# Kernel optimization log

Measured on AMD Instinct MI355X. Metric: run time of the kernel, lower is better.

Reference implementation:

```python
import jax, jax.numpy as jnp
import numpy as np

D, DFFN, H, P, L = 256, 1024, 8, 4, 4
B, LQ = 32, 300
LENS = [2048, 1024, 512, 256]
STARTS = [0, 2048, 3072, 3584]
S = sum(LENS)


def setup_inputs() -> dict:
    key = jax.random.key(0)
    ks = iter(jax.random.split(key, 64))
    def W(shape, s=0.02):
        return jax.random.normal(next(ks), shape, jnp.float32) * s
    inp = {}
    inp['tgt'] = W((B, LQ, D), 1.0)
    inp['query_pos'] = W((B, LQ, D), 1.0)
    centers = jax.random.uniform(next(ks), (B, LQ, L))
    widths = 0.05 + 0.2 * jax.random.uniform(next(ks), (B, LQ, L))
    inp['reference_points'] = jnp.stack([centers, widths], -1)  # (B,Lq,L,2) = (center,width)
    inp['src'] = W((B, S, D), 1.0)
    inp['temporal_lengths'] = np.array(LENS, np.int64)
    inp['level_start_index'] = np.array(STARTS, np.int64)
    for n, shape in [('sa_qw', (D, D)), ('sa_kw', (D, D)), ('sa_vw', (D, D)), ('sa_ow', (D, D)), ('ff1_w', (D, DFFN)), ('ff2_w', (DFFN, D))]:
        inp[n] = W(shape)
    for n, sz in [('sa_qb', D), ('sa_kb', D), ('sa_vb', D), ('sa_ob', D), ('ff1_b', DFFN), ('ff2_b', D)]:
        inp[n] = jnp.zeros((sz,), jnp.float32)
    for pre in ['ca', 'se']:
        inp[pre + '_off_w'] = W((D, H * L * P))
        inp[pre + '_off_b'] = jnp.zeros((H * L * P,), jnp.float32)
        inp[pre + '_attn_w'] = W((D, H * L * P))
        inp[pre + '_attn_b'] = jnp.zeros((H * L * P,), jnp.float32)
        inp[pre + '_val_w'] = W((D, D))
        inp[pre + '_val_b'] = jnp.zeros((D,), jnp.float32)
        inp[pre + '_out_w'] = W((D, D))
        inp[pre + '_out_b'] = jnp.zeros((D,), jnp.float32)
    for n in ['ln1', 'lnse', 'ln2', 'ln3']:
        inp[n + '_g'] = jnp.ones((D,), jnp.float32)
        inp[n + '_b'] = jnp.zeros((D,), jnp.float32)
    return inp


def _ln(x, g, b, eps=1e-5):
    m = jnp.mean(x, -1, keepdims=True)
    v = jnp.mean((x - m) ** 2, -1, keepdims=True)
    return (x - m) * jax.lax.rsqrt(v + eps) * g + b


def _mha(q, k, v, qw, qb, kw, kb, vw, vb, ow, ob):
    b, lq, d = q.shape
    dh = d // H
    qh = (q @ qw + qb).reshape(b, lq, H, dh).transpose(0, 2, 1, 3)
    kh = (k @ kw + kb).reshape(b, -1, H, dh).transpose(0, 2, 1, 3)
    vh = (v @ vw + vb).reshape(b, -1, H, dh).transpose(0, 2, 1, 3)
    scores = jnp.einsum('bhqd,bhkd->bhqk', qh, kh) * (dh ** -0.5)
    attn = jax.nn.softmax(scores, -1)
    out = jnp.einsum('bhqk,bhkd->bhqd', attn, vh).transpose(0, 2, 1, 3).reshape(b, lq, d)
    return out @ ow + ob


def _deform(q, ref, src, lens, starts, vw, vb, offw, offb, aw, ab, ow, ob, boundary):
    b, lq, d = q.shape
    dh = d // H
    value = (src @ vw + vb).reshape(b, -1, H, dh)  # (B,S,H,Dh)
    off = (q @ offw + offb).reshape(b, lq, H, L, P)
    attn = jax.nn.softmax((q @ aw + ab).reshape(b, lq, H, L * P), -1).reshape(b, lq, H, L, P)
    center = ref[..., 0][:, :, None, :, None]  # (B,Lq,1,L,1)
    width = ref[..., 1][:, :, None, :, None]
    if boundary:
        # half the points anchored at segment start, half at segment end
        sign = jnp.where(jnp.arange(P) < P // 2, -0.5, 0.5)
        anchor = center + sign * width
    else:
        anchor = center
    loc = anchor + off / P * width * 0.5  # normalized sampling locations (B,Lq,H,L,P)
    out = jnp.zeros((b, lq, H, dh), value.dtype)
    for l in range(L):
        T = int(lens[l]); s0 = int(starts[l])
        v = value[:, s0:s0 + T].transpose(0, 2, 1, 3)  # (B,H,T,Dh)
        x = loc[:, :, :, l, :] * T - 0.5  # align_corners=False grid
        x0 = jnp.floor(x)
        w = x - x0
        i0 = x0.astype(jnp.int32)
        i1 = i0 + 1
        m0 = ((i0 >= 0) & (i0 < T)).astype(v.dtype)
        m1 = ((i1 >= 0) & (i1 < T)).astype(v.dtype)
        i0c = jnp.clip(i0, 0, T - 1)
        i1c = jnp.clip(i1, 0, T - 1)
        def gather(idx):
            idxh = idx.transpose(0, 2, 1, 3).reshape(b, H, lq * P, 1)
            g = jnp.take_along_axis(v, jnp.broadcast_to(idxh, (b, H, lq * P, dh)), axis=2)
            return g.reshape(b, H, lq, P, dh).transpose(0, 2, 1, 3, 4)  # (B,Lq,H,P,Dh)
        samp = gather(i0c) * ((1 - w) * m0)[..., None] + gather(i1c) * (w * m1)[..., None]
        out = out + jnp.einsum('bqhp,bqhpd->bqhd', attn[:, :, :, l, :], samp)
    return out.reshape(b, lq, d) @ ow + ob


def reference(tgt, query_pos, reference_points, src, temporal_lengths, level_start_index,
              sa_qw, sa_qb, sa_kw, sa_kb, sa_vw, sa_vb, sa_ow, sa_ob,
              ca_off_w, ca_off_b, ca_attn_w, ca_attn_b, ca_val_w, ca_val_b, ca_out_w, ca_out_b,
              se_off_w, se_off_b, se_attn_w, se_attn_b, se_val_w, se_val_b, se_out_w, se_out_b,
              ff1_w, ff1_b, ff2_w, ff2_b,
              ln1_g, ln1_b, lnse_g, lnse_b, ln2_g, ln2_b, ln3_g, ln3_b):
    lens = np.asarray(temporal_lengths)
    starts = np.asarray(level_start_index)
    q = tgt + query_pos
    t2 = _mha(q, q, tgt, sa_qw, sa_qb, sa_kw, sa_kb, sa_vw, sa_vb, sa_ow, sa_ob)
    tgt = _ln(tgt + t2, ln2_g, ln2_b)
    t2 = _deform(tgt + query_pos, reference_points, src, lens, starts,
                 ca_val_w, ca_val_b, ca_off_w, ca_off_b, ca_attn_w, ca_attn_b, ca_out_w, ca_out_b, False)
    tgt = _ln(tgt + t2, ln1_g, ln1_b)
    t2 = _deform(tgt + query_pos, reference_points, src, lens, starts,
                 se_val_w, se_val_b, se_off_w, se_off_b, se_attn_w, se_attn_b, se_out_w, se_out_b, True)
    tgt = _ln(tgt + t2, lnse_g, lnse_b)
    t2 = jax.nn.relu(tgt @ ff1_w + ff1_b) @ ff2_w + ff2_b
    tgt = _ln(tgt + t2, ln3_g, ln3_b)
    return tgt
```

## Files before the change

### kernel.cpp

```cpp
#include <hip/hip_runtime.h>
#include <hip/hip_bf16.h>

namespace {

typedef unsigned short u16;
typedef unsigned int u32;

constexpr int D    = 256;
constexpr int H    = 8;
constexpr int DH   = 32;
constexpr int B    = 32;
constexpr int LQ   = 300;
constexpr int NQ   = B * LQ;
constexpr int S    = 3840;
constexpr int MS   = B * S;
constexpr int DFFN = 1024;

typedef __attribute__((ext_vector_type(8))) short bf16x8;
typedef __attribute__((ext_vector_type(4))) float f32x4;

__device__ inline u16 f2b(float x) {
  u32 u = __builtin_bit_cast(u32, x);
  u32 r = (u + 0x7FFFu + ((u >> 16) & 1u)) >> 16;
  return (u16)r;
}
__device__ inline u32 pk2(float a, float b) {
  return (u32)f2b(a) | ((u32)f2b(b) << 16);
}
__device__ inline void unpack2(u32 w, float& a, float& b) {
  a = __builtin_bit_cast(float, w << 16);
  b = __builtin_bit_cast(float, w & 0xffff0000u);
}

template<bool BOUNDARY>
__device__ inline void deform_phase(
    int tid, int m0,
    const float* __restrict__ oa, const float* __restrict__ ref,
    const u16* __restrict__ value, uint4* owt , char* Ast)
{
#pragma unroll
  for (int qq = 0; qq < 8; ++qq) {
    const int ql = (tid >> 7) + 4 * qq;
    const int bq = m0 + ql;
    const int t  = tid & 127;
    const int h = t >> 4;
    const int l = (t >> 2) & 3;
    const int p = t & 3;

    const float off    = oa[(size_t)bq * 256 + t];
    const float logit  = oa[(size_t)bq * 256 + 128 + t];
    const float center = ref[(size_t)bq * 8 + l * 2 + 0];
    const float width  = ref[(size_t)bq * 8 + l * 2 + 1];

    const float e = __expf(logit);
    float ssum = e;
    ssum += __shfl_xor(ssum, 1, 64);
    ssum += __shfl_xor(ssum, 2, 64);
    ssum += __shfl_xor(ssum, 4, 64);
    ssum += __shfl_xor(ssum, 8, 64);
    const float wa = e / ssum;

    const int T  = 2048 >> l;
    const int s0 = 4096 - (4096 >> l);
    float anchor = center;
    if (BOUNDARY) anchor += (p < 2 ? -0.5f : 0.5f) * width;
    const float loc = anchor + off * width * 0.125f;
    const float x = loc * (float)T - 0.5f;
    const float x0 = floorf(x);
    const float w = x - x0;
    const int i0 = (int)x0;
    const int i1 = i0 + 1;
    const float w0 = (i0 >= 0 && i0 < T) ? wa * (1.f - w) : 0.f;
    const float w1 = (i1 >= 0 && i1 < T) ? wa * w : 0.f;
    const int i0c = min(max(i0, 0), T - 1);
    const int i1c = min(max(i1, 0), T - 1);
    uint4 pack;
    pack.x = (u32)((h * S + s0 + i0c) * (DH * 2));
    pack.y = __builtin_bit_cast(u32, w0);
    pack.z = (u32)((h * S + s0 + i1c) * (DH * 2));
    pack.w = __builtin_bit_cast(u32, w1);
    owt[ql * 128 + t] = pack;
  }
  __syncthreads();

#pragma unroll
  for (int qq = 0; qq < 8; ++qq) {
    const int ql = (tid >> 7) + 4 * qq;
    const int bq = m0 + ql;
    const int b = bq / LQ;
    const int t = tid & 127;
    const int g  = t >> 4;
    const int ln = t & 15;
    const int qd = ln & 3;
    const int ts = ln >> 2;
    const char* vb = (const char*)(value + (size_t)b * H * S * DH) + qd * 16;
    float o[8] = {};
#pragma unroll
    for (int i = 0; i < 8; ++i) {
      const int rowidx = i * 4 + ts;
      const uint4 ow = owt[ql * 128 + g * 16 + (rowidx >> 1)];
      const u32 boff = (rowidx & 1) ? ow.z : ow.x;
      const float wt = __builtin_bit_cast(float, (rowidx & 1) ? ow.w : ow.y);
      const uint4 v = *(const uint4*)(vb + boff);
      float a0, a1;
      unpack2(v.x, a0, a1); o[0] += wt * a0; o[1] += wt * a1;
      unpack2(v.y, a0, a1); o[2] += wt * a0; o[3] += wt * a1;
      unpack2(v.z, a0, a1); o[4] += wt * a0; o[5] += wt * a1;
      unpack2(v.w, a0, a1); o[6] += wt * a0; o[7] += wt * a1;
    }
#pragma unroll
    for (int d = 0; d < 8; ++d) {
      o[d] += __shfl_xor(o[d], 4, 64);
      o[d] += __shfl_xor(o[d], 8, 64);
    }
    if (ts == 0) {
      const int col = g * DH + qd * 8;
      uint4 wv;
      wv.x = pk2(o[0], o[1]); wv.y = pk2(o[2], o[3]);
      wv.z = pk2(o[4], o[5]); wv.w = pk2(o[6], o[7]);
      *(uint4*)(Ast + ql * 512 + ((col * 2) ^ ((ql & 7) << 4))) = wv;
    }
  }
  __syncthreads();
}

__global__ __launch_bounds__(256) void gemm_qkv(
    const u16* __restrict__ qbuf, const u16* __restrict__ tgtb,
    const u16* __restrict__ saqk_t, const u16* __restrict__ sav_t,
    const float* __restrict__ qkb, const float* __restrict__ vbias,
    u16* __restrict__ qkbuf, u16* __restrict__ vh)
{
  constexpr int K = 256, BK = 64, LDK = 72;
  __shared__ __align__(16) u16 sh[128 * LDK];
  u16* As = sh;
  u16* Bs = sh + 64 * LDK;
  const bool isv = blockIdx.x >= 8;
  const u16* A  = isv ? tgtb : qbuf;
  const u16* Bt = isv ? sav_t : saqk_t;
  const float* bias = isv ? vbias : qkb;
  u16* C = isv ? vh : qkbuf;
  const int N = isv ? 256 : 512;
  const int n0 = (isv ? (int)blockIdx.x - 8 : (int)blockIdx.x) * 64;
  const int m0 = blockIdx.y * 64;

  const int tid  = threadIdx.x;
  const int lane = tid & 63;
  const int wid  = tid >> 6;
  const int wm = wid >> 1, wn = wid & 1;

  f32x4 acc[2][2] = {};
  uint4 ra[2], rb[2];
  const int srow = tid >> 3, sch = (tid & 7) * 8;

#pragma unroll
  for (int i = 0; i < 2; ++i) {
    const int row = srow + i * 32;
    ra[i] = *(const uint4*)(A  + (size_t)(m0 + row) * K + sch);
    rb[i] = *(const uint4*)(Bt + (size_t)(n0 + row) * K + sch);
  }
  for (int t = 0; t < 4; ++t) {
#pragma unroll
    for (int i = 0; i < 2; ++i) {
      const int row = srow + i * 32;
      *(uint4*)(&As[row * LDK + sch]) = ra[i];
      *(uint4*)(&Bs[row * LDK + sch]) = rb[i];
    }
    __syncthreads();
    if (t + 1 < 4) {
      const int k0 = (t + 1) * BK;
#pragma unroll
      for (int i = 0; i < 2; ++i) {
        const int row = srow + i * 32;
        ra[i] = *(const uint4*)(A  + (size_t)(m0 + row) * K + k0 + sch);
        rb[i] = *(const uint4*)(Bt + (size_t)(n0 + row) * K + k0 + sch);
      }
    }
#pragma unroll
    for (int kk = 0; kk < 2; ++kk) {
      const int krd = kk * 32 + (lane >> 4) * 8;
      bf16x8 af[2], bf[2];
#pragma unroll
      for (int m = 0; m < 2; ++m)
        af[m] = *(const bf16x8*)(&As[(wm * 32 + (lane & 15) + 16 * m) * LDK + krd]);
#pragma unroll
      for (int n = 0; n < 2; ++n)
        bf[n] = *(const bf16x8*)(&Bs[(wn * 32 + (lane & 15) + 16 * n) * LDK + krd]);
#pragma unroll
      for (int m = 0; m < 2; ++m)
#pragma unroll
        for (int n = 0; n < 2; ++n)
          acc[m][n] = __builtin_amdgcn_mfma_f32_16x16x32_bf16(af[m], bf[n], acc[m][n], 0, 0, 0);
    }
    __syncthreads();
  }

  const int cr = (lane >> 4) * 4;
  const int cc = lane & 15;
  u16* stg = sh;
#pragma unroll
  for (int n = 0; n < 2; ++n) {
    const int lc = wn * 32 + n * 16 + cc;
    const float bv = bias[n0 + lc];
#pragma unroll
    for (int m = 0; m < 2; ++m) {
      const int lr0 = wm * 32 + m * 16 + cr;
#pragma unroll
      for (int r = 0; r < 4; ++r)
        stg[(lr0 + r) * LDK + lc] = f2b(acc[m][n][r] + bv);
    }
  }
  __syncthreads();
#pragma unroll
  for (int i = 0; i < 2; ++i) {
    const int c = tid + 256 * i;
    const int row = c >> 3, ch = c & 7;
    *(uint4*)(C + (size_t)(m0 + row) * N + n0 + ch * 8) =
        *(const uint4*)(&stg[row * LDK + ch * 8]);
  }
}

__global__ __launch_bounds__(512) void gemm_val4(
    const float* __restrict__ A, const u16* __restrict__ Bt2,
    const float* __restrict__ bias2, u16* __restrict__ Vca, u16* __restrict__ Vse)
{
  __shared__ __align__(16) char shraw[33792];
  char* Asw = shraw;
  const int tid  = threadIdx.x;
  const int lane = tid & 63;
  const int w    = tid >> 6;
  const int bid  = blockIdx.x;
  const int nh   = (bid >> 3) & 1;
  const int m0   = ((bid >> 4) * 8 + (bid & 7)) * 64;
  u16* dst = nh ? Vse : Vca;
  const u16* Bt = Bt2 + nh * 256 * 256;
  const float* bias = bias2 + nh * 256;
  const int b  = m0 / S;
  const int s0 = m0 - b * S;

#pragma unroll
  for (int i = 0; i < 4; ++i) {
    const int idx = tid + 512 * i;
    const int row = idx >> 5, ch = idx & 31;
    const float* ap = A + (size_t)(m0 + row) * 256 + ch * 8;
    const float4 f0 = *(const float4*)(ap);
    const float4 f1 = *(const float4*)(ap + 4);
    uint4 pk;
    pk.x = pk2(f0.x, f0.y); pk.y = pk2(f0.z, f0.w);
    pk.z = pk2(f1.x, f1.y); pk.w = pk2(f1.z, f1.w);
    *(uint4*)(Asw + row * 512 + ((ch * 16) ^ ((row & 7) << 4))) = pk;
  }
  __syncthreads();

  f32x4 acc[4][2] = {};
  const u16* bb = Bt + (size_t)(w * 32 + (lane & 15)) * 256 + (lane >> 4) * 8;
  bf16x8 bcur[2], bnxt[2];
#pragma unroll
  for (int n = 0; n < 2; ++n) bcur[n] = *(const bf16x8*)(bb + n * 4096);

#pragma unroll
  for (int kk = 0; kk < 8; ++kk) {
    bf16x8 af[4];
    const int kb = kk * 64 + (lane >> 4) * 16;
#pragma unroll
    for (int m = 0; m < 4; ++m) {
      const int row = m * 16 + (lane & 15);
      af[m] = *(const bf16x8*)(Asw + row * 512 + (kb ^ ((row & 7) << 4)));
    }
    if (kk < 7) {
#pragma unroll
      for (int n = 0; n < 2; ++n)
        bnxt[n] = *(const bf16x8*)(bb + n * 4096 + (kk + 1) * 32);
    }
#pragma unroll
    for (int m = 0; m < 4; ++m)
#pragma unroll
      for (int n = 0; n < 2; ++n)
        acc[m][n] = __builtin_amdgcn_mfma_f32_16x16x32_bf16(af[m], bcur[n], acc[m][n], 0, 0, 0);
#pragma unroll
    for (int n = 0; n < 2; ++n) bcur[n] = bnxt[n];
  }
  __syncthreads();

  constexpr int STC = 264;
  u16* stg = (u16*)shraw;
  const int cr = (lane >> 4) * 4;
  const int cc = lane & 15;
#pragma unroll
  for (int n = 0; n < 2; ++n) {
    const int col = w * 32 + n * 16 + cc;
    const float bv = bias[col];
#pragma unroll
    for (int m = 0; m < 4; ++m) {
      const int r0 = m * 16 + cr;
#pragma unroll
      for (int r = 0; r < 4; ++r)
        stg[(r0 + r) * STC + col] = f2b(acc[m][n][r] + bv);
    }
  }
  __syncthreads();
  u16* vb = dst + (size_t)b * H * S * DH;
#pragma unroll
  for (int i = 0; i < 4; ++i) {
    const int c = tid + 512 * i;
    const int row = c >> 5, ch = c & 31;
    const int h = ch >> 2, dq = ch & 3;
    *(uint4*)(vb + ((size_t)h * S + (s0 + row)) * DH + dq * 8) =
        *(const uint4*)(&stg[row * STC + ch * 8]);
  }
}

__global__ __launch_bounds__(1024) void gemm_lnoff(
    const u16* __restrict__ A, const u16* __restrict__ Bt,
    const float* __restrict__ bias, const float* __restrict__ res,
    const float* __restrict__ g, const float* __restrict__ be,
    const float* __restrict__ qpos,
    const u16* __restrict__ offw, const float* __restrict__ offb,
    float* __restrict__ fout, float* __restrict__ oaout)
{
  constexpr int K = 256, LDK = 72;
  __shared__ __align__(16) float ftile[64 * 264];
  u16* As = (u16*)ftile;
  u16* Bs = As + 64 * LDK;
  u16* aq = (u16*)ftile;
  const int tid  = threadIdx.x;
  const int lane = tid & 63;
  const int wid  = tid >> 6;
  const int wm = wid >> 2, wn = wid & 3;
  const int m0 = blockIdx.x * 64;

  f32x4 acc[4] = {};
  const bool am = tid < 512;
  const int arow = tid >> 3, ach = (tid & 7) * 8;

  uint4 ra = {};
  uint4 rb[2];
  if (am) ra = *(const uint4*)(A + (size_t)(m0 + arow) * K + ach);
#pragma unroll
  for (int i = 0; i < 2; ++i) {
    const int idx = tid + 1024 * i;
    const int brow = idx >> 3, bch = (idx & 7) * 8;
    rb[i] = *(const uint4*)(Bt + (size_t)brow * K + bch);
  }

  for (int t = 0; t < 4; ++t) {
    if (am) *(uint4*)(&As[arow * LDK + ach]) = ra;
#pragma unroll
    for (int i = 0; i < 2; ++i) {
      const int idx = tid + 1024 * i;
      const int brow = idx >> 3, bch = (idx & 7) * 8;
      *(uint4*)(&Bs[brow * LDK + bch]) = rb[i];
    }
    __syncthreads();
    if (t + 1 < 4) {
      const int k0 = (t + 1) * 64;
      if (am) ra = *(const uint4*)(A + (size_t)(m0 + arow) * K + k0 + ach);
#pragma unroll
      for (int i = 0; i < 2; ++i) {
        const int idx = tid + 1024 * i;
        const int brow = idx >> 3, bch = (idx & 7) * 8;
        rb[i] = *(const uint4*)(Bt + (size_t)brow * K + k0 + bch);
      }
    }
#pragma unroll
    for (int kk = 0; kk < 2; ++kk) {
      const int krd = kk * 32 + (lane >> 4) * 8;
      bf16x8 af, bf[4];
      af = *(const bf16x8*)(&As[(wm * 16 + (lane & 15)) * LDK + krd]);
#pragma unroll
      for (int n = 0; n < 4; ++n)
        bf[n] = *(const bf16x8*)(&Bs[(wn * 64 + n * 16 + (lane & 15)) * LDK + krd]);
#pragma unroll
      for (int n = 0; n < 4; ++n)
        acc[n] = __builtin_amdgcn_mfma_f32_16x16x32_bf16(af, bf[n], acc[n], 0, 0, 0);
    }
    __syncthreads();
  }

  const int cr = (lane >> 4) * 4;
  const int cc = lane & 15;
#pragma unroll
  for (int n = 0; n < 4; ++n) {
    const int col = wn * 64 + n * 16 + cc;
    const float bv = bias[col];
#pragma unroll
    for (int r = 0; r < 4; ++r)
      ftile[(wm * 16 + cr + r) * 264 + col] = acc[n][r] + bv;
  }
  __syncthreads();

  const int row = tid >> 4, s16 = tid & 15;
  const size_t grow = (size_t)(m0 + row) * 256;
  float vv[16];
  float sum = 0.f;
#pragma unroll
  for (int j = 0; j < 4; ++j) {
    const int col = s16 * 4 + j * 64;
    const float4 fv = *(const float4*)(&ftile[row * 264 + col]);
    const float4 rv = *(const float4*)(res + grow + col);
    vv[j * 4 + 0] = fv.x + rv.x; vv[j * 4 + 1] = fv.y + rv.y;
    vv[j * 4 + 2] = fv.z + rv.z; vv[j * 4 + 3] = fv.w + rv.w;
    sum += vv[j * 4 + 0] + vv[j * 4 + 1] + vv[j * 4 + 2] + vv[j * 4 + 3];
  }
  sum += __shfl_xor(sum, 1, 64);
  sum += __shfl_xor(sum, 2, 64);
  sum += __shfl_xor(sum, 4, 64);
  sum += __shfl_xor(sum, 8, 64);
  const float mean = sum * (1.f / 256.f);
  float sq = 0.f;
#pragma unroll
  for (int k = 0; k < 16; ++k) { const float d = vv[k] - mean; sq += d * d; }
  sq += __shfl_xor(sq, 1, 64);
  sq += __shfl_xor(sq, 2, 64);
  sq += __shfl_xor(sq, 4, 64);
  sq += __shfl_xor(sq, 8, 64);
  const float rstd = rsqrtf(sq * (1.f / 256.f) + 1e-5f);

  float yq[16];
#pragma unroll
  for (int j = 0; j < 4; ++j) {
    const int col = s16 * 4 + j * 64;
    const float4 gv = *(const float4*)(g + col);
    const float4 bv = *(const float4*)(be + col);
    const float4 qv = *(const float4*)(qpos + grow + col);
    float4 y;
    y.x = (vv[j * 4 + 0] - mean) * rstd * gv.x + bv.x;
    y.y = (vv[j * 4 + 1] - mean) * rstd * gv.y + bv.y;
    y.z = (vv[j * 4 + 2] - mean) * rstd * gv.z + bv.z;
    y.w = (vv[j * 4 + 3] - mean) * rstd * gv.w + bv.w;
    *(float4*)(fout + grow + col) = y;
    yq[j * 4 + 0] = y.x + qv.x; yq[j * 4 + 1] = y.y + qv.y;
    yq[j * 4 + 2] = y.z + qv.z; yq[j * 4 + 3] = y.w + qv.w;
  }
  __syncthreads();

#pragma unroll
  for (int j = 0; j < 4; ++j) {
    const int col = s16 * 4 + j * 64;
    uint2 pk;
    pk.x = pk2(yq[j * 4 + 0], yq[j * 4 + 1]);
    pk.y = pk2(yq[j * 4 + 2], yq[j * 4 + 3]);
    *(uint2*)(&aq[row * 264 + col]) = pk;
  }
  __syncthreads();

  f32x4 acc2[4] = {};
  const u16* bb = offw + (size_t)(wn * 64 + (lane & 15)) * 256 + (lane >> 4) * 8;
#pragma unroll
  for (int kk = 0; kk < 8; ++kk) {
    const bf16x8 af = *(const bf16x8*)(&aq[(wm * 16 + (lane & 15)) * 264 + kk * 32 + (lane >> 4) * 8]);
#pragma unroll
    for (int n = 0; n < 4; ++n) {
      const bf16x8 bf = *(const bf16x8*)(bb + (size_t)n * 16 * 256 + kk * 32);
      acc2[n] = __builtin_amdgcn_mfma_f32_16x16x32_bf16(af, bf, acc2[n], 0, 0, 0);
    }
  }
  __syncthreads();

#pragma unroll
  for (int n = 0; n < 4; ++n) {
    const int col = wn * 64 + n * 16 + cc;
    const float bv = offb[col];
#pragma unroll
    for (int r = 0; r < 4; ++r)
      ftile[(wm * 16 + cr + r) * 264 + col] = acc2[n][r] + bv;
  }
  __syncthreads();
#pragma unroll
  for (int i = 0; i < 4; ++i) {
    const int c = tid + 1024 * i;
    const int rw = c >> 6, ch = c & 63;
    *(float4*)(oaout + (size_t)(m0 + rw) * 256 + ch * 4) =
        *(const float4*)(&ftile[rw * 264 + ch * 4]);
  }
}

__global__ __launch_bounds__(512) void deform_lnoff(
    const float* __restrict__ oa, const float* __restrict__ ref,
    const u16* __restrict__ value,
    const u16* __restrict__ Wout, const float* __restrict__ bout,
    const float* __restrict__ res, const float* __restrict__ g,
    const float* __restrict__ be, const float* __restrict__ qpos,
    const u16* __restrict__ offw, const float* __restrict__ offb,
    float* __restrict__ fout, float* __restrict__ oaout)
{
  __shared__ __align__(16) char sh[81920];
  char* Ast = sh;
  uint4* owt = (uint4*)(sh + 16384);
  float* ftile = (float*)sh;
  u16* aq = (u16*)sh;
  const int tid  = threadIdx.x;
  const int lane = tid & 63;
  const int w    = tid >> 6;
  const int m0   = blockIdx.x * 32;
  const int cr = (lane >> 4) * 4;
  const int cc = lane & 15;

  deform_phase<false>(tid, m0, oa, ref, value, owt, Ast);

  f32x4 accB[2][2] = {};
  {
    const u16* bb = Wout + (size_t)(w * 32 + (lane & 15)) * 256 + (lane >> 4) * 8;
#pragma unroll
    for (int kk = 0; kk < 8; ++kk) {
      bf16x8 af[2];
      const int kb = kk * 64 + (lane >> 4) * 16;
#pragma unroll
      for (int m = 0; m < 2; ++m) {
        const int row = m * 16 + (lane & 15);
        af[m] = *(const bf16x8*)(Ast + row * 512 + (kb ^ ((row & 7) << 4)));
      }
#pragma unroll
      for (int n = 0; n < 2; ++n) {
        const bf16x8 bf = *(const bf16x8*)(bb + (size_t)n * 16 * 256 + kk * 32);
#pragma unroll
        for (int m = 0; m < 2; ++m)
          accB[m][n] = __builtin_amdgcn_mfma_f32_16x16x32_bf16(af[m], bf, accB[m][n], 0, 0, 0);
      }
    }
  }
  __syncthreads();

#pragma unroll
  for (int n = 0; n < 2; ++n) {
    const int col = w * 32 + n * 16 + cc;
    const float bv = bout[col];
#pragma unroll
    for (int m = 0; m < 2; ++m)
#pragma unroll
      for (int r = 0; r < 4; ++r)
        ftile[(m * 16 + cr + r) * 264 + col] = accB[m][n][r] + bv;
  }
  __syncthreads();

  const int row = tid >> 4, s16 = tid & 15;
  const size_t grow = (size_t)(m0 + row) * 256;
  float yq[16];
  {
    float vv[16];
    float sum = 0.f;
#pragma unroll
    for (int j = 0; j < 4; ++j) {
      const int col = s16 * 4 + j * 64;
      const float4 fv = *(const float4*)(&ftile[row * 264 + col]);
      const float4 rv = *(const float4*)(res + grow + col);
      vv[j * 4 + 0] = fv.x + rv.x; vv[j * 4 + 1] = fv.y + rv.y;
      vv[j * 4 + 2] = fv.z + rv.z; vv[j * 4 + 3] = fv.w + rv.w;
      sum += vv[j * 4 + 0] + vv[j * 4 + 1] + vv[j * 4 + 2] + vv[j * 4 + 3];
    }
    sum += __shfl_xor(sum, 1, 64);
    sum += __shfl_xor(sum, 2, 64);
    sum += __shfl_xor(sum, 4, 64);
    sum += __shfl_xor(sum, 8, 64);
    const float mean = sum * (1.f / 256.f);
    float sq = 0.f;
#pragma unroll
    for (int k = 0; k < 16; ++k) { const float d = vv[k] - mean; sq += d * d; }
    sq += __shfl_xor(sq, 1, 64);
    sq += __shfl_xor(sq, 2, 64);
    sq += __shfl_xor(sq, 4, 64);
    sq += __shfl_xor(sq, 8, 64);
    const float rstd = rsqrtf(sq * (1.f / 256.f) + 1e-5f);
#pragma unroll
    for (int j = 0; j < 4; ++j) {
      const int col = s16 * 4 + j * 64;
      const float4 gv = *(const float4*)(g + col);
      const float4 bv = *(const float4*)(be + col);
      const float4 qv = *(const float4*)(qpos + grow + col);
      float4 y;
      y.x = (vv[j * 4 + 0] - mean) * rstd * gv.x + bv.x;
      y.y = (vv[j * 4 + 1] - mean) * rstd * gv.y + bv.y;
      y.z = (vv[j * 4 + 2] - mean) * rstd * gv.z + bv.z;
      y.w = (vv[j * 4 + 3] - mean) * rstd * gv.w + bv.w;
      *(float4*)(fout + grow + col) = y;
      yq[j * 4 + 0] = y.x + qv.x; yq[j * 4 + 1] = y.y + qv.y;
      yq[j * 4 + 2] = y.z + qv.z; yq[j * 4 + 3] = y.w + qv.w;
    }
  }
  __syncthreads();

#pragma unroll
  for (int j = 0; j < 4; ++j) {
    const int col = s16 * 4 + j * 64;
    uint2 pk;
    pk.x = pk2(yq[j * 4 + 0], yq[j * 4 + 1]);
    pk.y = pk2(yq[j * 4 + 2], yq[j * 4 + 3]);
    *(uint2*)(&aq[row * 264 + col]) = pk;
  }
  __syncthreads();

  f32x4 acc2[2][2] = {};
  {
    const u16* bb = offw + (size_t)(w * 32 + (lane & 15)) * 256 + (lane >> 4) * 8;
#pragma unroll
    for (int kk = 0; kk < 8; ++kk) {
      bf16x8 af[2];
#pragma unroll
      for (int m = 0; m < 2; ++m)
        af[m] = *(const bf16x8*)(&aq[(m * 16 + (lane & 15)) * 264 + kk * 32 + (lane >> 4) * 8]);
#pragma unroll
      for (int n = 0; n < 2; ++n) {
        const bf16x8 bf = *(const bf16x8*)(bb + (size_t)n * 16 * 256 + kk * 32);
#pragma unroll
        for (int m = 0; m < 2; ++m)
          acc2[m][n] = __builtin_amdgcn_mfma_f32_16x16x32_bf16(af[m], bf, acc2[m][n], 0, 0, 0);
      }
    }
  }
  __syncthreads();

#pragma unroll
  for (int n = 0; n < 2; ++n) {
    const int col = w * 32 + n * 16 + cc;
    const float bv = offb[col];
#pragma unroll
    for (int m = 0; m < 2; ++m)
#pragma unroll
      for (int r = 0; r < 4; ++r)
        ftile[(m * 16 + cr + r) * 264 + col] = acc2[m][n][r] + bv;
  }
  __syncthreads();
#pragma unroll
  for (int i = 0; i < 4; ++i) {
    const int c = tid + 512 * i;
    const int rw = c >> 6, ch = c & 63;
    *(float4*)(oaout + (size_t)(m0 + rw) * 256 + ch * 4) =
        *(const float4*)(&ftile[rw * 264 + ch * 4]);
  }
}

__global__ __launch_bounds__(512) void gemm_tail2(
    const float* __restrict__ oa, const float* __restrict__ ref,
    const u16* __restrict__ value,
    const u16* __restrict__ Wout, const float* __restrict__ bout,
    const float* __restrict__ res,
    const float* __restrict__ g1, const float* __restrict__ be1,
    const u16* __restrict__ B1t, const u16* __restrict__ B2t,
    const float* __restrict__ b1, const float* __restrict__ b2,
    const float* __restrict__ g2, const float* __restrict__ be2,
    float* __restrict__ fout)
{
  __shared__ __align__(16) char sh[81920];
  char* Ast = sh;
  uint4* owt = (uint4*)(sh + 16384);
  char* ffh = sh + 16384;
  float* ftile = (float*)sh;
  const int tid  = threadIdx.x;
  const int lane = tid & 63;
  const int w    = tid >> 6;
  const int m0   = blockIdx.x * 32;
  const int cr = (lane >> 4) * 4;
  const int cc = lane & 15;

  deform_phase<true>(tid, m0, oa, ref, value, owt, Ast);

  f32x4 accB[2][2] = {};
  {
    const u16* bb = Wout + (size_t)(w * 32 + (lane & 15)) * 256 + (lane >> 4) * 8;
#pragma unroll
    for (int kk = 0; kk < 8; ++kk) {
      bf16x8 af[2];
      const int kb = kk * 64 + (lane >> 4) * 16;
#pragma unroll
      for (int m = 0; m < 2; ++m) {
        const int row = m * 16 + (lane & 15);
        af[m] = *(const bf16x8*)(Ast + row * 512 + (kb ^ ((row & 7) << 4)));
      }
#pragma unroll
      for (int n = 0; n < 2; ++n) {
        const bf16x8 bf = *(const bf16x8*)(bb + (size_t)n * 16 * 256 + kk * 32);
#pragma unroll
        for (int m = 0; m < 2; ++m)
          accB[m][n] = __builtin_amdgcn_mfma_f32_16x16x32_bf16(af[m], bf, accB[m][n], 0, 0, 0);
      }
    }
  }
  __syncthreads();

#pragma unroll
  for (int n = 0; n < 2; ++n) {
    const int col = w * 32 + n * 16 + cc;
    const float bv = bout[col];
#pragma unroll
    for (int m = 0; m < 2; ++m)
#pragma unroll
      for (int r = 0; r < 4; ++r)
        ftile[(m * 16 + cr + r) * 264 + col] = accB[m][n][r] + bv;
  }
  __syncthreads();

  const int row = tid >> 4, s16 = tid & 15;
  const size_t grow = (size_t)(m0 + row) * 256;
  float yv[16];
  {
    float vv[16];
    float sum = 0.f;
#pragma unroll
    for (int j = 0; j < 4; ++j) {
      const int col = s16 * 4 + j * 64;
      const float4 fv = *(const float4*)(&ftile[row * 264 + col]);
      const float4 rv = *(const float4*)(res + grow + col);
      vv[j * 4 + 0] = fv.x + rv.x; vv[j * 4 + 1] = fv.y + rv.y;
      vv[j * 4 + 2] = fv.z + rv.z; vv[j * 4 + 3] = fv.w + rv.w;
      sum += vv[j * 4 + 0] + vv[j * 4 + 1] + vv[j * 4 + 2] + vv[j * 4 + 3];
    }
    sum += __shfl_xor(sum, 1, 64);
    sum += __shfl_xor(sum, 2, 64);
    sum += __shfl_xor(sum, 4, 64);
    sum += __shfl_xor(sum, 8, 64);
    const float mean = sum * (1.f / 256.f);
    float sq = 0.f;
#pragma unroll
    for (int k = 0; k < 16; ++k) { const float d = vv[k] - mean; sq += d * d; }
    sq += __shfl_xor(sq, 1, 64);
    sq += __shfl_xor(sq, 2, 64);
    sq += __shfl_xor(sq, 4, 64);
    sq += __shfl_xor(sq, 8, 64);
    const float rstd = rsqrtf(sq * (1.f / 256.f) + 1e-5f);
#pragma unroll
    for (int j = 0; j < 4; ++j) {
      const int col = s16 * 4 + j * 64;
      const float4 gv = *(const float4*)(g1 + col);
      const float4 bv = *(const float4*)(be1 + col);
      yv[j * 4 + 0] = (vv[j * 4 + 0] - mean) * rstd * gv.x + bv.x;
      yv[j * 4 + 1] = (vv[j * 4 + 1] - mean) * rstd * gv.y + bv.y;
      yv[j * 4 + 2] = (vv[j * 4 + 2] - mean) * rstd * gv.z + bv.z;
      yv[j * 4 + 3] = (vv[j * 4 + 3] - mean) * rstd * gv.w + bv.w;
    }
  }
  __syncthreads();

#pragma unroll
  for (int j = 0; j < 4; ++j) {
    const int col = s16 * 4 + j * 64;
    uint2 pk;
    pk.x = pk2(yv[j * 4 + 0], yv[j * 4 + 1]);
    pk.y = pk2(yv[j * 4 + 2], yv[j * 4 + 3]);
    *(uint2*)(Ast + row * 512 + ((col * 2) ^ ((row & 7) << 4))) = pk;
  }
  __syncthreads();

  {
    f32x4 acc[2][8] = {};
    const u16* bb = B1t + (size_t)(w * 128 + (lane & 15)) * 256 + (lane >> 4) * 8;
#pragma unroll
    for (int kk = 0; kk < 8; ++kk) {
      bf16x8 af[2];
      const int kb = kk * 64 + (lane >> 4) * 16;
#pragma unroll
      for (int m = 0; m < 2; ++m) {
        const int rw = m * 16 + (lane & 15);
        af[m] = *(const bf16x8*)(Ast + rw * 512 + (kb ^ ((rw & 7) << 4)));
      }
#pragma unroll
      for (int n = 0; n < 8; ++n) {
        const bf16x8 bf = *(const bf16x8*)(bb + (size_t)n * 16 * 256 + kk * 32);
#pragma unroll
        for (int m = 0; m < 2; ++m)
          acc[m][n] = __builtin_amdgcn_mfma_f32_16x16x32_bf16(af[m], bf, acc[m][n], 0, 0, 0);
      }
    }
#pragma unroll
    for (int n = 0; n < 8; ++n) {
      const int col = w * 128 + n * 16 + cc;
      const float bv = b1[col];
#pragma unroll
      for (int m = 0; m < 2; ++m) {
#pragma unroll
        for (int r = 0; r < 4; ++r) {
          const int rw = m * 16 + cr + r;
          const float x = fmaxf(acc[m][n][r] + bv, 0.f);
          *(u16*)(ffh + rw * 2048 + ((col * 2) ^ ((rw & 7) << 4))) = f2b(x);
        }
      }
    }
  }
  __syncthreads();

  f32x4 acc2[2][2] = {};
  {
    const u16* bb = B2t + (size_t)(w * 32 + (lane & 15)) * 1024 + (lane >> 4) * 8;
#pragma unroll 4
    for (int kk = 0; kk < 32; ++kk) {
      bf16x8 af[2];
      const int kb = kk * 64 + (lane >> 4) * 16;
#pragma unroll
      for (int m = 0; m < 2; ++m) {
        const int rw = m * 16 + (lane & 15);
        af[m] = *(const bf16x8*)(ffh + rw * 2048 + (kb ^ ((rw & 7) << 4)));
      }
#pragma unroll
      for (int n = 0; n < 2; ++n) {
        const bf16x8 bf = *(const bf16x8*)(bb + (size_t)n * 16 * 1024 + kk * 32);
#pragma unroll
        for (int m = 0; m < 2; ++m)
          acc2[m][n] = __builtin_amdgcn_mfma_f32_16x16x32_bf16(af[m], bf, acc2[m][n], 0, 0, 0);
      }
    }
  }
  __syncthreads();

#pragma unroll
  for (int n = 0; n < 2; ++n) {
    const int col = w * 32 + n * 16 + cc;
    const float bv = b2[col];
#pragma unroll
    for (int m = 0; m < 2; ++m)
#pragma unroll
      for (int r = 0; r < 4; ++r)
        ftile[(m * 16 + cr + r) * 264 + col] = acc2[m][n][r] + bv;
  }
  __syncthreads();

  {
    float vv[16];
    float sum = 0.f;
#pragma unroll
    for (int j = 0; j < 4; ++j) {
      const int col = s16 * 4 + j * 64;
      const float4 fv = *(const float4*)(&ftile[row * 264 + col]);
      vv[j * 4 + 0] = fv.x + yv[j * 4 + 0]; vv[j * 4 + 1] = fv.y + yv[j * 4 + 1];
      vv[j * 4 + 2] = fv.z + yv[j * 4 + 2]; vv[j * 4 + 3] = fv.w + yv[j * 4 + 3];
      sum += vv[j * 4 + 0] + vv[j * 4 + 1] + vv[j * 4 + 2] + vv[j * 4 + 3];
    }
    sum += __shfl_xor(sum, 1, 64);
    sum += __shfl_xor(sum, 2, 64);
    sum += __shfl_xor(sum, 4, 64);
    sum += __shfl_xor(sum, 8, 64);
    const float mean = sum * (1.f / 256.f);
    float sq = 0.f;
#pragma unroll
    for (int k = 0; k < 16; ++k) { const float d = vv[k] - mean; sq += d * d; }
    sq += __shfl_xor(sq, 1, 64);
    sq += __shfl_xor(sq, 2, 64);
    sq += __shfl_xor(sq, 4, 64);
    sq += __shfl_xor(sq, 8, 64);
    const float rstd = rsqrtf(sq * (1.f / 256.f) + 1e-5f);
#pragma unroll
    for (int j = 0; j < 4; ++j) {
      const int col = s16 * 4 + j * 64;
      const float4 gv = *(const float4*)(g2 + col);
      const float4 bv = *(const float4*)(be2 + col);
      float4 y;
      y.x = (vv[j * 4 + 0] - mean) * rstd * gv.x + bv.x;
      y.y = (vv[j * 4 + 1] - mean) * rstd * gv.y + bv.y;
      y.z = (vv[j * 4 + 2] - mean) * rstd * gv.z + bv.z;
      y.w = (vv[j * 4 + 3] - mean) * rstd * gv.w + bv.w;
      *(float4*)(fout + grow + col) = y;
    }
  }
}

struct WSpec { const float* w; u16* wt; int K, N, blk0; };
struct WPack { WSpec s[14]; };

struct PrepArgs {
  const float *ca_off_b, *ca_attn_b, *se_off_b, *se_attn_b;
  const float *sa_qb, *sa_kb, *ca_val_b, *se_val_b;
  float *bias4, *qkb, *valb;
  const float *tgt, *qpos;
  u16 *tgtb, *qbuf;
  int n4, nwt;
};

__global__ __launch_bounds__(256) void prep_all(WPack p, PrepArgs a) {
  __shared__ float tile[32][33];
  const int b = blockIdx.x;
  if (b < a.nwt) {
    int i = 0;
#pragma unroll
    for (int j = 1; j < 14; ++j) if (b >= p.s[j].blk0) i = j;
    const float* w = p.s[i].w;
    u16* wt = p.s[i].wt;
    const int K = p.s[i].K, N = p.s[i].N;
    const int lb = b - p.s[i].blk0;
    const int ntN = N >> 5;
    const int tk = lb / ntN, tn = lb - tk * ntN;
    const int r = threadIdx.x >> 5, c = threadIdx.x & 31;
#pragma unroll
    for (int j = 0; j < 4; ++j)
      tile[r + j * 8][c] = w[(size_t)(tk * 32 + r + j * 8) * N + tn * 32 + c];
    __syncthreads();
#pragma unroll
    for (int j = 0; j < 4; ++j)
      wt[(size_t)(tn * 32 + r + j * 8) * K + tk * 32 + c] = f2b(tile[c][r + j * 8]);
  } else if (b == a.nwt) {
#pragma unroll
    for (int u = 0; u < 2; ++u) {
      const int t = threadIdx.x + 256 * u;
      a.bias4[t] = t < 128 ? a.ca_off_b[t] : t < 256 ? a.ca_attn_b[t - 128]
                 : t < 384 ? a.se_off_b[t - 256] : a.se_attn_b[t - 384];
      a.qkb[t]  = t < 256 ? a.sa_qb[t] : a.sa_kb[t - 256];
      a.valb[t] = t < 256 ? a.ca_val_b[t] : a.se_val_b[t - 256];
    }
  } else {
    const int i = (b - a.nwt - 1) * 256 + threadIdx.x;
    if (i < a.n4) {
      const float4 t = ((const float4*)a.tgt)[i];
      const float4 q = ((const float4*)a.qpos)[i];
      uint2 x, y;
      x.x = pk2(t.x, t.y); x.y = pk2(t.z, t.w);
      y.x = pk2(t.x + q.x, t.y + q.y); y.y = pk2(t.z + q.z, t.w + q.w);
      ((uint2*)a.tgtb)[i] = x;
      ((uint2*)a.qbuf)[i] = y;
    }
  }
}

__global__ __launch_bounds__(512) void mha_v2(
    const u16* __restrict__ qk, const u16* __restrict__ vh,
    u16* __restrict__ out)
{
  __shared__ __align__(16) float Ks[8 * 300 * 4];
  __shared__ __align__(16) float Vs[8 * 300 * 4];
  const int bh  = blockIdx.x & 255;
  const int seg = blockIdx.x >> 8;
  const int b = bh >> 3, h = bh & 7;
  const u16* kbase = qk + (size_t)b * LQ * 512 + 256 + h * DH;
  const u16* vbase = vh + (size_t)b * LQ * D + h * DH;
  for (int e = threadIdx.x; e < 300 * 8; e += 512) {
    const int r = e >> 3, j = e & 7;
    float4 f;
    const uint2 kv = *(const uint2*)(kbase + (size_t)r * 512 + j * 4);
    unpack2(kv.x, f.x, f.y);
    unpack2(kv.y, f.z, f.w);
    *(float4*)(&Ks[(j * 300 + r) * 4]) = f;
    const uint2 vv = *(const uint2*)(vbase + (size_t)r * D + j * 4);
    unpack2(vv.x, f.x, f.y);
    unpack2(vv.y, f.z, f.w);
    *(float4*)(&Vs[(j * 300 + r) * 4]) = f;
  }
  __syncthreads();

  const int lane = threadIdx.x & 63;
  const int lq = (threadIdx.x >> 6) * 16 + (lane >> 2);
  const int kc = lane & 3;
  const int q = seg * 128 + lq;
  if (q >= LQ) return;

  const u16* qrow = qk + (size_t)(b * LQ + q) * 512 + h * DH;
  float qv[DH];
#pragma unroll
  for (int c4 = 0; c4 < 4; ++c4) {
    const uint4 u = *(const uint4*)(qrow + c4 * 8);
    unpack2(u.x, qv[c4 * 8 + 0], qv[c4 * 8 + 1]);
    unpack2(u.y, qv[c4 * 8 + 2], qv[c4 * 8 + 3]);
    unpack2(u.z, qv[c4 * 8 + 4], qv[c4 * 8 + 5]);
    unpack2(u.w, qv[c4 * 8 + 6], qv[c4 * 8 + 7]);
  }
#pragma unroll
  for (int d = 0; d < DH; ++d) qv[d] *= 0.17677669529663689f;

  float o[DH] = {};
  float ssum = 0.f;
  const float* kp = &Ks[kc * 75 * 4];
  const float* vp = &Vs[kc * 75 * 4];
  for (int i = 0; i < 75; ++i) {
    float s = 0.f;
#pragma unroll
    for (int j = 0; j < 8; ++j) {
      const float4 kf = *(const float4*)(kp + i * 4 + j * 1200);
      s += qv[j * 4 + 0] * kf.x + qv[j * 4 + 1] * kf.y
         + qv[j * 4 + 2] * kf.z + qv[j * 4 + 3] * kf.w;
    }
    const float p = __expf(s);
    ssum += p;
#pragma unroll
    for (int j = 0; j < 8; ++j) {
      const float4 vf = *(const float4*)(vp + i * 4 + j * 1200);
      o[j * 4 + 0] += p * vf.x; o[j * 4 + 1] += p * vf.y;
      o[j * 4 + 2] += p * vf.z; o[j * 4 + 3] += p * vf.w;
    }
  }

  ssum += __shfl_xor(ssum, 1, 64);
  ssum += __shfl_xor(ssum, 2, 64);
#pragma unroll
  for (int d = 0; d < DH; ++d) {
    o[d] += __shfl_xor(o[d], 1, 64);
    o[d] += __shfl_xor(o[d], 2, 64);
  }
  const float inv = 1.f / ssum;

  u16* orow = out + (size_t)(b * LQ + q) * D + h * DH;
#pragma unroll
  for (int c = 0; c < 4; ++c) {
    if (kc == c) {
      uint4 w;
      w.x = pk2(o[c * 8 + 0] * inv, o[c * 8 + 1] * inv);
      w.y = pk2(o[c * 8 + 2] * inv, o[c * 8 + 3] * inv);
      w.z = pk2(o[c * 8 + 4] * inv, o[c * 8 + 5] * inv);
      w.w = pk2(o[c * 8 + 6] * inv, o[c * 8 + 7] * inv);
      *(uint4*)(orow + c * 8) = w;
    }
  }
}

}

extern "C" void kernel_launch(void* const* d_in, const int* in_sizes, int n_in,
                              void* d_out, int out_size, void* d_ws, size_t ws_size,
                              hipStream_t stream)
{
  const float* tgt   = (const float*)d_in[0];
  const float* qpos  = (const float*)d_in[1];
  const float* ref   = (const float*)d_in[2];
  const float* src   = (const float*)d_in[3];
  const float* sa_qw = (const float*)d_in[6];
  const float* sa_kw = (const float*)d_in[7];
  const float* sa_vw = (const float*)d_in[8];
  const float* sa_ow = (const float*)d_in[9];
  const float* ff1_w = (const float*)d_in[10];
  const float* ff2_w = (const float*)d_in[11];
  const float* sa_qb = (const float*)d_in[12];
  const float* sa_kb = (const float*)d_in[13];
  const float* sa_vb = (const float*)d_in[14];
  const float* sa_ob = (const float*)d_in[15];
  const float* ff1_b = (const float*)d_in[16];
  const float* ff2_b = (const float*)d_in[17];
  const float* ca_off_w  = (const float*)d_in[18];
  const float* ca_off_b  = (const float*)d_in[19];
  const float* ca_attn_w = (const float*)d_in[20];
  const float* ca_attn_b = (const float*)d_in[21];
  const float* ca_val_w  = (const float*)d_in[22];
  const float* ca_val_b  = (const float*)d_in[23];
  const float* ca_out_w  = (const float*)d_in[24];
  const float* ca_out_b  = (const float*)d_in[25];
  const float* se_off_w  = (const float*)d_in[26];
  const float* se_off_b  = (const float*)d_in[27];
  const float* se_attn_w = (const float*)d_in[28];
  const float* se_attn_b = (const float*)d_in[29];
  const float* se_val_w  = (const float*)d_in[30];
  const float* se_val_b  = (const float*)d_in[31];
  const float* se_out_w  = (const float*)d_in[32];
  const float* se_out_b  = (const float*)d_in[33];
  const float* ln1_g  = (const float*)d_in[34];
  const float* ln1_b  = (const float*)d_in[35];
  const float* lnse_g = (const float*)d_in[36];
  const float* lnse_b = (const float*)d_in[37];
  const float* ln2_g  = (const float*)d_in[38];
  const float* ln2_b  = (const float*)d_in[39];
  const float* ln3_g  = (const float*)d_in[40];
  const float* ln3_b  = (const float*)d_in[41];

  const size_t ND = (size_t)NQ * D;
  const size_t MD = (size_t)MS * D;

  char* base = (char*)d_ws;
  size_t off = 0;
  auto alloc = [&](size_t bytes) -> void* {
    void* p = base + off;
    off += (bytes + 255) & ~(size_t)255;
    return p;
  };
  u16*  Vca  = (u16*)alloc(MD * 2);
  u16*  Vse  = (u16*)alloc(MD * 2);
  u16*  qkbuf = (u16*)alloc((size_t)NQ * 512 * 2);
  u16*  vh   = (u16*)alloc(ND * 2);
  u16*  qbuf = (u16*)alloc(ND * 2);
  u16*  smpb = (u16*)alloc(ND * 2);
  u16*  tgtb = (u16*)alloc(ND * 2);
  float* cur = (float*)alloc(ND * 4);
  float* oabuf = (float*)alloc((size_t)NQ * 256 * 4);
  float* bias4 = (float*)alloc(512 * 4);
  float* qkb   = (float*)alloc(512 * 4);
  float* valb  = (float*)alloc(512 * 4);

  WPack pk;
  int wi = 0, blk = 0;
  auto addw = [&](const float* w, int K, int N) -> u16* {
    u16* wt = (u16*)alloc((size_t)K * N * 2);
    pk.s[wi].w = w; pk.s[wi].wt = wt; pk.s[wi].K = K; pk.s[wi].N = N; pk.s[wi].blk0 = blk;
    blk += (K / 32) * (N / 32);
    ++wi;
    return wt;
  };
  u16* saq_t = addw(sa_qw, D, D);
  u16* sak_t = addw(sa_kw, D, D);        (void)sak_t;
  u16* sav_t = addw(sa_vw, D, D);
  u16* sao_t = addw(sa_ow, D, D);
  u16* ff1_t = addw(ff1_w, D, DFFN);
  u16* ff2_t = addw(ff2_w, DFFN, D);
  u16* caoff_t = addw(ca_off_w, D, 128);
  u16* caatt_t = addw(ca_attn_w, D, 128);  (void)caatt_t;
  u16* seoff_t = addw(se_off_w, D, 128);
  u16* seatt_t = addw(se_attn_w, D, 128);  (void)seatt_t;
  u16* caval_t = addw(ca_val_w, D, D);
  u16* seval_t = addw(se_val_w, D, D);     (void)seval_t;
  u16* caout_t = addw(ca_out_w, D, D);
  u16* seout_t = addw(se_out_w, D, D);

  const int n4 = (int)(ND / 4);

  PrepArgs pa;
  pa.ca_off_b = ca_off_b; pa.ca_attn_b = ca_attn_b;
  pa.se_off_b = se_off_b; pa.se_attn_b = se_attn_b;
  pa.sa_qb = sa_qb; pa.sa_kb = sa_kb; pa.ca_val_b = ca_val_b; pa.se_val_b = se_val_b;
  pa.bias4 = bias4; pa.qkb = qkb; pa.valb = valb;
  pa.tgt = tgt; pa.qpos = qpos; pa.tgtb = tgtb; pa.qbuf = qbuf;
  pa.n4 = n4; pa.nwt = blk;
  prep_all<<<blk + 1 + 2400, 256, 0, stream>>>(pk, pa);

  gemm_val4<<<(MS / 64) * 2, 512, 0, stream>>>(src, caval_t, valb, Vca, Vse);

  gemm_qkv<<<dim3(12, 150), 256, 0, stream>>>(qbuf, tgtb, saq_t, sav_t, qkb, sa_vb, qkbuf, vh);
  mha_v2<<<B * H * 3, 512, 0, stream>>>(qkbuf, vh, smpb);
  gemm_lnoff<<<NQ / 64, 1024, 0, stream>>>(smpb, sao_t, sa_ob, tgt, ln2_g, ln2_b,
                                           qpos, caoff_t, bias4, cur, oabuf);

  deform_lnoff<<<NQ / 32, 512, 0, stream>>>(oabuf, ref, Vca,
                                            caout_t, ca_out_b, cur, ln1_g, ln1_b,
                                            qpos, seoff_t, bias4 + 256, cur, oabuf);

  gemm_tail2<<<NQ / 32, 512, 0, stream>>>(oabuf, ref, Vse,
                                          seout_t, se_out_b, cur,
                                          lnse_g, lnse_b, ff1_t, ff2_t,
                                          ff1_b, ff2_b, ln3_g, ln3_b,
                                          (float*)d_out);
}
```

Baseline: 416.5 us.

## Shrink LDS footprint by chunking deform sampling and FFN hidden dimension

The deformable-sampling phase now processes 8 queries at a time instead of 32, so the offset/weight table needs a quarter of the shared memory. The FFN in the tail kernel is split into four 256-wide hidden chunks, each computing FF1 then accumulating into FF2, so the hidden buffer shrinks from 2048 to 512 bytes per row. Together these cut LDS from 80KB to 33KB per block, and launch bounds now request 6 blocks per CU, aiming to raise occupancy and hide gather latency. The cost is more __syncthreads barriers and possible register pressure from the tighter launch bound.

```diff
diff --git a/kernel.cpp b/kernel.cpp
--- a/kernel.cpp
+++ b/kernel.cpp
@@ -33,15 +33,15 @@
 }
 
 template<bool BOUNDARY>
-__device__ inline void deform_phase(
-    int tid, int m0,
+__device__ inline void deform_phase8(
+    int tid, int m0, int q0,
     const float* __restrict__ oa, const float* __restrict__ ref,
     const u16* __restrict__ value, uint4* owt , char* Ast)
 {
 #pragma unroll
-  for (int qq = 0; qq < 8; ++qq) {
-    const int ql = (tid >> 7) + 4 * qq;
-    const int bq = m0 + ql;
+  for (int qq = 0; qq < 2; ++qq) {
+    const int qr = (tid >> 7) + 4 * qq;
+    const int bq = m0 + q0 + qr;
     const int t  = tid & 127;
     const int h = t >> 4;
     const int l = (t >> 2) & 3;
@@ -79,13 +79,14 @@
     pack.y = __builtin_bit_cast(u32, w0);
     pack.z = (u32)((h * S + s0 + i1c) * (DH * 2));
     pack.w = __builtin_bit_cast(u32, w1);
-    owt[ql * 128 + t] = pack;
-  }
-  __syncthreads();
-
-#pragma unroll
-  for (int qq = 0; qq < 8; ++qq) {
-    const int ql = (tid >> 7) + 4 * qq;
+    owt[qr * 128 + t] = pack;
+  }
+  __syncthreads();
+
+#pragma unroll
+  for (int qq = 0; qq < 2; ++qq) {
+    const int qr = (tid >> 7) + 4 * qq;
+    const int ql = q0 + qr;
     const int bq = m0 + ql;
     const int b = bq / LQ;
     const int t = tid & 127;
@@ -98,7 +99,7 @@
 #pragma unroll
     for (int i = 0; i < 8; ++i) {
       const int rowidx = i * 4 + ts;
-      const uint4 ow = owt[ql * 128 + g * 16 + (rowidx >> 1)];
+      const uint4 ow = owt[qr * 128 + g * 16 + (rowidx >> 1)];
       const u32 boff = (rowidx & 1) ? ow.z : ow.x;
       const float wt = __builtin_bit_cast(float, (rowidx & 1) ? ow.w : ow.y);
       const uint4 v = *(const uint4*)(vb + boff);
@@ -474,7 +475,7 @@
   }
 }
 
-__global__ __launch_bounds__(512) void deform_lnoff(
+__global__ __launch_bounds__(512, 6) void deform_lnoff(
     const float* __restrict__ oa, const float* __restrict__ ref,
     const u16* __restrict__ value,
     const u16* __restrict__ Wout, const float* __restrict__ bout,
@@ -483,7 +484,7 @@
     const u16* __restrict__ offw, const float* __restrict__ offb,
     float* __restrict__ fout, float* __restrict__ oaout)
 {
-  __shared__ __align__(16) char sh[81920];
+  __shared__ __align__(16) char sh[33792];
   char* Ast = sh;
   uint4* owt = (uint4*)(sh + 16384);
   float* ftile = (float*)sh;
@@ -495,7 +496,8 @@
   const int cr = (lane >> 4) * 4;
   const int cc = lane & 15;
 
-  deform_phase<false>(tid, m0, oa, ref, value, owt, Ast);
+  for (int q0 = 0; q0 < 32; q0 += 8)
+    deform_phase8<false>(tid, m0, q0, oa, ref, value, owt, Ast);
 
   f32x4 accB[2][2] = {};
   {
@@ -628,7 +630,7 @@
   }
 }
 
-__global__ __launch_bounds__(512) void gemm_tail2(
+__global__ __launch_bounds__(512, 6) void gemm_tail2(
     const float* __restrict__ oa, const float* __restrict__ ref,
     const u16* __restrict__ value,
     const u16* __restrict__ Wout, const float* __restrict__ bout,
@@ -639,7 +641,7 @@
     const float* __restrict__ g2, const float* __restrict__ be2,
     float* __restrict__ fout)
 {
-  __shared__ __align__(16) char sh[81920];
+  __shared__ __align__(16) char sh[33792];
   char* Ast = sh;
   uint4* owt = (uint4*)(sh + 16384);
   char* ffh = sh + 16384;
@@ -651,7 +653,8 @@
   const int cr = (lane >> 4) * 4;
   const int cc = lane & 15;
 
-  deform_phase<true>(tid, m0, oa, ref, value, owt, Ast);
+  for (int q0 = 0; q0 < 32; q0 += 8)
+    deform_phase8<true>(tid, m0, q0, oa, ref, value, owt, Ast);
 
   f32x4 accB[2][2] = {};
   {
@@ -739,65 +742,67 @@
   }
   __syncthreads();
 
-  {
-    f32x4 acc[2][8] = {};
-    const u16* bb = B1t + (size_t)(w * 128 + (lane & 15)) * 256 + (lane >> 4) * 8;
-#pragma unroll
-    for (int kk = 0; kk < 8; ++kk) {
-      bf16x8 af[2];
-      const int kb = kk * 64 + (lane >> 4) * 16;
-#pragma unroll
-      for (int m = 0; m < 2; ++m) {
-        const int rw = m * 16 + (lane & 15);
-        af[m] = *(const bf16x8*)(Ast + rw * 512 + (kb ^ ((rw & 7) << 4)));
-      }
-#pragma unroll
-      for (int n = 0; n < 8; ++n) {
-        const bf16x8 bf = *(const bf16x8*)(bb + (size_t)n * 16 * 256 + kk * 32);
-#pragma unroll
-        for (int m = 0; m < 2; ++m)
-          acc[m][n] = __builtin_amdgcn_mfma_f32_16x16x32_bf16(af[m], bf, acc[m][n], 0, 0, 0);
-      }
-    }
-#pragma unroll
-    for (int n = 0; n < 8; ++n) {
-      const int col = w * 128 + n * 16 + cc;
-      const float bv = b1[col];
-#pragma unroll
-      for (int m = 0; m < 2; ++m) {
-#pragma unroll
-        for (int r = 0; r < 4; ++r) {
-          const int rw = m * 16 + cr + r;
-          const float x = fmaxf(acc[m][n][r] + bv, 0.f);
-          *(u16*)(ffh + rw * 2048 + ((col * 2) ^ ((rw & 7) << 4))) = f2b(x);
+  f32x4 acc2[2][2] = {};
+  for (int hf = 0; hf < 4; ++hf) {
+    {
+      f32x4 acc1[2][2] = {};
+      const u16* bb = B1t + (size_t)(hf * 256 + w * 32 + (lane & 15)) * 256 + (lane >> 4) * 8;
+#pragma unroll
+      for (int kk = 0; kk < 8; ++kk) {
+        bf16x8 af[2];
+        const int kb = kk * 64 + (lane >> 4) * 16;
+#pragma unroll
+        for (int m = 0; m < 2; ++m) {
+          const int rw = m * 16 + (lane & 15);
+          af[m] = *(const bf16x8*)(Ast + rw * 512 + (kb ^ ((rw & 7) << 4)));
+        }
+#pragma unroll
+        for (int n = 0; n < 2; ++n) {
+          const bf16x8 bf = *(const bf16x8*)(bb + (size_t)n * 16 * 256 + kk * 32);
+#pragma unroll
+          for (int m = 0; m < 2; ++m)
+            acc1[m][n] = __builtin_amdgcn_mfma_f32_16x16x32_bf16(af[m], bf, acc1[m][n], 0, 0, 0);
         }
       }
-    }
-  }
-  __syncthreads();
-
-  f32x4 acc2[2][2] = {};
-  {
-    const u16* bb = B2t + (size_t)(w * 32 + (lane & 15)) * 1024 + (lane >> 4) * 8;
-#pragma unroll 4
-    for (int kk = 0; kk < 32; ++kk) {
-      bf16x8 af[2];
-      const int kb = kk * 64 + (lane >> 4) * 16;
-#pragma unroll
-      for (int m = 0; m < 2; ++m) {
-        const int rw = m * 16 + (lane & 15);
-        af[m] = *(const bf16x8*)(ffh + rw * 2048 + (kb ^ ((rw & 7) << 4)));
+#pragma unroll
+      for (int n = 0; n < 2; ++n) {
+        const int lcol = w * 32 + n * 16 + cc;
+        const float bv = b1[hf * 256 + lcol];
+#pragma unroll
+        for (int m = 0; m < 2; ++m) {
+#pragma unroll
+          for (int r = 0; r < 4; ++r) {
+            const int rw = m * 16 + cr + r;
+            const float x = fmaxf(acc1[m][n][r] + bv, 0.f);
+            *(u16*)(ffh + rw * 512 + ((lcol * 2) ^ ((rw & 7) << 4))) = f2b(x);
+          }
+        }
       }
-#pragma unroll
-      for (int n = 0; n < 2; ++n) {
-        const bf16x8 bf = *(const bf16x8*)(bb + (size_t)n * 16 * 1024 + kk * 32);
-#pragma unroll
-        for (int m = 0; m < 2; ++m)
-          acc2[m][n] = __builtin_amdgcn_mfma_f32_16x16x32_bf16(af[m], bf, acc2[m][n], 0, 0, 0);
+    }
+    __syncthreads();
+
+    {
+      const u16* bb = B2t + (size_t)(w * 32 + (lane & 15)) * 1024 + (lane >> 4) * 8;
+#pragma unroll
+      for (int kk = 0; kk < 8; ++kk) {
+        bf16x8 af[2];
+        const int kb = kk * 64 + (lane >> 4) * 16;
+#pragma unroll
+        for (int m = 0; m < 2; ++m) {
+          const int rw = m * 16 + (lane & 15);
+          af[m] = *(const bf16x8*)(ffh + rw * 512 + (kb ^ ((rw & 7) << 4)));
+        }
+#pragma unroll
+        for (int n = 0; n < 2; ++n) {
+          const bf16x8 bf = *(const bf16x8*)(bb + (size_t)n * 16 * 1024 + (hf * 8 + kk) * 32);
+#pragma unroll
+          for (int m = 0; m < 2; ++m)
+            acc2[m][n] = __builtin_amdgcn_mfma_f32_16x16x32_bf16(af[m], bf, acc2[m][n], 0, 0, 0);
+        }
       }
     }
-  }
-  __syncthreads();
+    __syncthreads();
+  }
 
 #pragma unroll
   for (int n = 0; n < 2; ++n) {
```

After: 426.3 us. 1.02x slower.
